# Optimization experiments

Measured on AMD Instinct MI355X. Metric: run time of the kernel, lower is better.

The kernel has to match this reference:

```python
import jax, jax.numpy as jnp
import numpy as np
import math

D = 2048
NH = 16
DH = D // NH
LAT = D // 4
B, S = 2, 2048
EPS = 1e-5


def _ln(x, g, b):
    m = jnp.mean(x, axis=-1, keepdims=True)
    v = jnp.mean((x - m) ** 2, axis=-1, keepdims=True)
    return (x - m) * jax.lax.rsqrt(v + EPS) * g + b


def setup_inputs() -> dict:
    key = jax.random.key(0)
    ks = jax.random.split(key, 12)
    p = lambda k, shape: 0.01 * jax.random.normal(k, shape, dtype=jnp.float32)
    return {
        "x": jax.random.normal(ks[0], (B, S, D), dtype=jnp.float32),
        "W_dq": p(ks[1], (D, LAT)),
        "W_uq": p(ks[2], (LAT, D)),
        "q_ln_g": jnp.ones((LAT,), jnp.float32),
        "q_ln_b": jnp.zeros((LAT,), jnp.float32),
        "W_dkv": p(ks[3], (D, LAT)),
        "W_ukv": p(ks[4], (LAT, 2 * D)),
        "kv_ln_g": jnp.ones((LAT,), jnp.float32),
        "kv_ln_b": jnp.zeros((LAT,), jnp.float32),
        "W_o": p(ks[5], (D, D)),
        "norm1_g": jnp.ones((D,), jnp.float32),
        "norm1_b": jnp.zeros((D,), jnp.float32),
        "norm2_g": jnp.ones((D,), jnp.float32),
        "norm2_b": jnp.zeros((D,), jnp.float32),
        "fc1_w": p(ks[6], (4 * D, D)),
        "fc1_b": jnp.zeros((4 * D,), jnp.float32),
        "fc2_w": p(ks[7], (D, 4 * D)),
        "fc2_b": jnp.zeros((D,), jnp.float32),
    }


def reference(x, W_dq, W_uq, q_ln_g, q_ln_b, W_dkv, W_ukv, kv_ln_g, kv_ln_b,
              W_o, norm1_g, norm1_b, norm2_g, norm2_b, fc1_w, fc1_b, fc2_w, fc2_b):
    normed = _ln(x, norm1_g, norm1_b)

    # --- RopelessMLA attention ---
    cq = _ln(normed @ W_dq, q_ln_g, q_ln_b)          # [B,S,LAT]
    Q = cq @ W_uq                                     # [B,S,D]
    ckv = _ln(normed @ W_dkv, kv_ln_g, kv_ln_b)       # [B,S,LAT]
    KV = ckv @ W_ukv                                  # [B,S,2D]
    K, V = KV[..., :D], KV[..., D:]

    q = Q.reshape(B, S, NH, DH)
    k = K.reshape(B, S, NH, DH)
    v = V.reshape(B, S, NH, DH)

    qkt = jnp.einsum("bqhd,bkhd->bhqk", q, k) / math.sqrt(float(DH))
    mask = jnp.tril(jnp.ones((S, S), dtype=qkt.dtype))  # causal, past_length=0
    qkt = qkt * mask
    qkt = jnp.where(qkt == 0.0, -jnp.inf, qkt)  # faithful to original zero->-inf trick
    attn = jax.nn.softmax(qkt, axis=-1)
    o = jnp.einsum("bhqk,bkhd->bqhd", attn, v).reshape(B, S, D)
    mh_x = o @ W_o.T

    x = x + mh_x
    h = _ln(x, norm2_g, norm2_b)
    h = jax.nn.relu(h @ fc1_w.T + fc1_b)
    h = h @ fc2_w.T + fc2_b  # dropout is identity in eval mode
    return x + h
```

## Files before the change

### kernel.cpp

```cpp
#include <hip/hip_runtime.h>
#include <hip/hip_bf16.h>


#define DEVI __device__ __forceinline__

typedef __attribute__((ext_vector_type(8))) short bf16x8;
typedef __attribute__((ext_vector_type(4))) float f32x4;

DEVI unsigned short f2bf(float f) {
  union { float f; unsigned u; } v; v.f = f;
  unsigned r = v.u + 0x7fffu + ((v.u >> 16) & 1u);
  return (unsigned short)(r >> 16);
}

DEVI float bf2f(unsigned short u) {
  union { unsigned u; float f; } v; v.u = ((unsigned)u) << 16;
  return v.f;
}

#define GLDS16(gp, lp)                                              \
  __builtin_amdgcn_global_load_lds(                                 \
      (__attribute__((address_space(1))) void*)(gp),                \
      (__attribute__((address_space(3))) void*)(lp), 16, 0, 0)

#define NEG_INF (-__builtin_inff())

__global__ __launch_bounds__(256) void cast_f32_bf16(
    const float* __restrict__ in, unsigned short* __restrict__ out, long n) {
  long i = ((long)blockIdx.x * 256 + threadIdx.x) * 4;
  if (i >= n) return;
  const float4 v = *reinterpret_cast<const float4*>(in + i);
  ushort4 o;
  o.x = f2bf(v.x); o.y = f2bf(v.y); o.z = f2bf(v.z); o.w = f2bf(v.w);
  *reinterpret_cast<ushort4*>(out + i) = o;
}

__global__ __launch_bounds__(256) void transpose_cast(
    const float* __restrict__ in, unsigned short* __restrict__ out, int R, int C) {
  __shared__ float tile[32][33];
  const int c0 = blockIdx.x * 32, r0 = blockIdx.y * 32;
  const int tx = threadIdx.x & 31, ty = threadIdx.x >> 5;
#pragma unroll
  for (int i = 0; i < 32; i += 8)
    tile[ty + i][tx] = in[(long)(r0 + ty + i) * C + c0 + tx];
  __syncthreads();
#pragma unroll
  for (int i = 0; i < 32; i += 8)
    out[(long)(c0 + ty + i) * R + r0 + tx] = f2bf(tile[tx][ty + i]);
}

__global__ __launch_bounds__(256) void v_transpose(
    const unsigned short* __restrict__ KV, unsigned short* __restrict__ Vt) {
  __shared__ unsigned short sh[32][33];
  const int s0 = blockIdx.x * 32, d0 = blockIdx.y * 32, bh = blockIdx.z;
  const int b = bh >> 4, h = bh & 15;
  const int tx = threadIdx.x & 31, ty = threadIdx.x >> 5;
#pragma unroll
  for (int i = 0; i < 32; i += 8)
    sh[ty + i][tx] = KV[((long)(b * 2048 + s0 + ty + i)) * 4096 + 2048 + h * 128 + d0 + tx];
  __syncthreads();
#pragma unroll
  for (int i = 0; i < 32; i += 8)
    Vt[((long)(bh * 128 + d0 + ty + i)) * 2048 + s0 + tx] = sh[tx][ty + i];
}

DEVI float blockReduceSum(float v) {
  v += __shfl_xor(v, 1);  v += __shfl_xor(v, 2);  v += __shfl_xor(v, 4);
  v += __shfl_xor(v, 8);  v += __shfl_xor(v, 16); v += __shfl_xor(v, 32);
  __shared__ float red[4];
  if ((threadIdx.x & 63) == 0) red[threadIdx.x >> 6] = v;
  __syncthreads();
  v = red[0] + red[1] + red[2] + red[3];
  __syncthreads();
  return v;
}

template <int W>
__global__ __launch_bounds__(256) void layernorm_bf16(
    const float* __restrict__ in, const float* __restrict__ g,
    const float* __restrict__ b, unsigned short* __restrict__ out, int ldin) {
  constexpr int VPT = W / 256;
  const long row = blockIdx.x;
  const float* x = in + row * ldin;
  float v[VPT];
  float s = 0.f;
#pragma unroll
  for (int i = 0; i < VPT; i++) { v[i] = x[threadIdx.x + i * 256]; s += v[i]; }
  s = blockReduceSum(s);
  const float mean = s * (1.0f / W);
  float s2 = 0.f;
#pragma unroll
  for (int i = 0; i < VPT; i++) { float d = v[i] - mean; s2 += d * d; }
  s2 = blockReduceSum(s2);
  const float rstd = rsqrtf(s2 * (1.0f / W) + 1e-5f);
#pragma unroll
  for (int i = 0; i < VPT; i++) {
    const int c = threadIdx.x + i * 256;
    out[row * W + c] = f2bf((v[i] - mean) * rstd * g[c] + b[c]);
  }
}

__global__ __launch_bounds__(256) void combine_ln(
    const unsigned short* __restrict__ p, const float* __restrict__ xres,
    const float* __restrict__ g, const float* __restrict__ b,
    float* __restrict__ x2, unsigned short* __restrict__ h1, long n) {
  const int c0 = threadIdx.x * 8;
  const long base = (long)blockIdx.x * 2048 + c0;
  float v[8];
  float s = 0.f;
#pragma unroll
  for (int hh = 0; hh < 2; hh++) {
    const long i = base + hh * 4;
    const ushort4 a  = *reinterpret_cast<const ushort4*>(p + i);
    const ushort4 bb = *reinterpret_cast<const ushort4*>(p + n + i);
    const float4 r = *reinterpret_cast<const float4*>(xres + i);
    float4 o;
    o.x = r.x + bf2f(a.x) + bf2f(bb.x);
    o.y = r.y + bf2f(a.y) + bf2f(bb.y);
    o.z = r.z + bf2f(a.z) + bf2f(bb.z);
    o.w = r.w + bf2f(a.w) + bf2f(bb.w);
    *reinterpret_cast<float4*>(x2 + i) = o;
    v[hh * 4 + 0] = o.x; v[hh * 4 + 1] = o.y;
    v[hh * 4 + 2] = o.z; v[hh * 4 + 3] = o.w;
    s += o.x + o.y + o.z + o.w;
  }
  s = blockReduceSum(s);
  const float mean = s * (1.0f / 2048.f);
  float s2 = 0.f;
#pragma unroll
  for (int i = 0; i < 8; i++) { float d = v[i] - mean; s2 += d * d; }
  s2 = blockReduceSum(s2);
  const float rstd = rsqrtf(s2 * (1.0f / 2048.f) + 1e-5f);
#pragma unroll
  for (int hh = 0; hh < 2; hh++) {
    const float4 gv = *reinterpret_cast<const float4*>(g + c0 + hh * 4);
    const float4 bv = *reinterpret_cast<const float4*>(b + c0 + hh * 4);
    ushort4 o;
    o.x = f2bf((v[hh * 4 + 0] - mean) * rstd * gv.x + bv.x);
    o.y = f2bf((v[hh * 4 + 1] - mean) * rstd * gv.y + bv.y);
    o.z = f2bf((v[hh * 4 + 2] - mean) * rstd * gv.z + bv.z);
    o.w = f2bf((v[hh * 4 + 3] - mean) * rstd * gv.w + bv.w);
    *reinterpret_cast<ushort4*>(h1 + base + hh * 4) = o;
  }
}

template <bool BIAS, bool RELU, bool RES, bool OBF16>
__global__ __launch_bounds__(256) void gemm_bt(
    const unsigned short* __restrict__ A, const unsigned short* __restrict__ Bt,
    const float* __restrict__ bias, const float* __restrict__ res,
    void* __restrict__ Cout, int M, int N, int K) {
  __shared__ __align__(16) unsigned short As[2][128 * 32];
  __shared__ __align__(16) unsigned short Bs[2][128 * 32];

  const int m0 = blockIdx.x * 128;
  const int n0 = blockIdx.y * 128;
  const int tid = threadIdx.x;
  const int lane = tid & 63, w = tid >> 6;
  const int wr = (w >> 1) * 64, wc = (w & 1) * 64;
  const int lrow = lane & 15, lk = (lane >> 4) * 8;

  f32x4 acc[4][4] = {};

  const int nt = K >> 5;
  const int r_ = (tid * 8) >> 5;
  const int c_ = (tid * 8) & 31;

#define STAGE(buf, t)                                                        \
  {                                                                          \
    const long k0 = (long)(t) * 32;                                          \
    GLDS16(A + (long)(m0 + r_) * K + k0 + c_, &As[buf][tid * 8]);            \
    GLDS16(A + (long)(m0 + 64 + r_) * K + k0 + c_, &As[buf][2048 + tid * 8]);\
    GLDS16(Bt + (long)(n0 + r_) * K + k0 + c_, &Bs[buf][tid * 8]);           \
    GLDS16(Bt + (long)(n0 + 64 + r_) * K + k0 + c_, &Bs[buf][2048 + tid * 8]);\
  }

  STAGE(0, 0)
  __syncthreads();
  int cur = 0;
  for (int t = 0; t < nt; t++) {
    if (t + 1 < nt) STAGE(cur ^ 1, t + 1)
    bf16x8 fa[4], fb[4];
#pragma unroll
    for (int i = 0; i < 4; i++) {
      fa[i] = *reinterpret_cast<const bf16x8*>(&As[cur][(wr + i * 16 + lrow) * 32 + lk]);
      fb[i] = *reinterpret_cast<const bf16x8*>(&Bs[cur][(wc + i * 16 + lrow) * 32 + lk]);
    }
#pragma unroll
    for (int i = 0; i < 4; i++)
#pragma unroll
      for (int j = 0; j < 4; j++)
        acc[i][j] = __builtin_amdgcn_mfma_f32_16x16x32_bf16(fa[i], fb[j], acc[i][j], 0, 0, 0);
    __syncthreads();
    cur ^= 1;
  }
#undef STAGE

#pragma unroll
  for (int i = 0; i < 4; i++) {
#pragma unroll
    for (int j = 0; j < 4; j++) {
      const int row = m0 + wr + i * 16 + ((lane >> 4) << 2);
      const int col = n0 + wc + j * 16 + lrow;
      float bv = 0.f;
      if (BIAS) bv = bias[col];
#pragma unroll
      for (int r = 0; r < 4; r++) {
        float v = acc[i][j][r];
        const long idx = (long)(row + r) * N + col;
        if (BIAS) v += bv;
        if (RELU) v = fmaxf(v, 0.f);
        if (RES) v += res[idx];
        if (OBF16) ((unsigned short*)Cout)[idx] = f2bf(v);
        else       ((float*)Cout)[idx] = v;
      }
    }
  }
}

template <bool BIAS, bool RELU, bool OBF16>
__global__ __launch_bounds__(512, 1) void gemm256p(
    const unsigned short* __restrict__ A, const unsigned short* __restrict__ Bt,
    const float* __restrict__ bias, void* __restrict__ Cout,
    int M, int N, int lda, int ldb, int kLen, long kOff) {
  __shared__ __align__(16) unsigned short L[2][2][2][256 * 32];

  const int m0 = blockIdx.x * 256, n0 = blockIdx.y * 256;
  const long ka = (long)blockIdx.z * kOff;
  const int tid = threadIdx.x;
  const int lane = tid & 63, w = tid >> 6;
  const int wm = w >> 2, wn = w & 3;
  const int g = lane >> 4, lrow = lane & 15;

  f32x4 acc[8][4] = {};
  const int nt = kLen >> 6;

#define STG(b, ab, kh, t, P, base0, ld)                                        \
  {                                                                            \
    const long k0 = ka + (long)(t) * 64 + (kh) * 32;                           \
    { const int o = tid;       const int r = o >> 2, s = o & 3;                \
      GLDS16((P) + (long)((base0) + r) * (ld) + k0 + ((s ^ ((r >> 1) & 3)) << 3), \
             &L[b][ab][kh][o * 8]); }                                          \
    { const int o = 512 + tid; const int r = o >> 2, s = o & 3;                \
      GLDS16((P) + (long)((base0) + r) * (ld) + k0 + ((s ^ ((r >> 1) & 3)) << 3), \
             &L[b][ab][kh][o * 8]); }                                          \
  }

#define RD_A(dst, Ahalf, qm)                                                   \
  _Pragma("unroll")                                                            \
  for (int i = 0; i < 4; i++) {                                                \
    const int r = wm * 128 + (qm) * 64 + i * 16 + lrow;                        \
    dst[i] = *reinterpret_cast<const bf16x8*>(                                 \
        &(Ahalf)[(r * 4 + (g ^ ((r >> 1) & 3))) * 8]);                         \
  }
#define RD_B(dst, Bhalf)                                                       \
  _Pragma("unroll")                                                            \
  for (int j = 0; j < 4; j++) {                                                \
    const int r = wn * 64 + j * 16 + lrow;                                     \
    dst[j] = *reinterpret_cast<const bf16x8*>(                                 \
        &(Bhalf)[(r * 4 + (g ^ ((r >> 1) & 3))) * 8]);                         \
  }

  STG(0, 0, 0, 0, A, m0, lda)
  STG(0, 1, 0, 0, Bt, n0, ldb)
  STG(0, 0, 1, 0, A, m0, lda)
  STG(0, 1, 1, 0, Bt, n0, ldb)
  asm volatile("s_waitcnt vmcnt(4)\n\ts_barrier" ::: "memory");

  for (int t = 0; t < nt; t++) {
    const int bu = t & 1, bn = bu ^ 1;
    const bool pf = (t + 1 < nt);
#pragma unroll
    for (int kh = 0; kh < 2; kh++) {
      const unsigned short* Ah = L[bu][0][kh];
      const unsigned short* Bh = L[bu][1][kh];
      bf16x8 fa[4], fa2[4], fb[4];
      RD_A(fa, Ah, 0)
      RD_B(fb, Bh)
      RD_A(fa2, Ah, 1)
      if (pf) {
        STG(bn, 0, kh, t + 1, A, m0, lda)
        STG(bn, 1, kh, t + 1, Bt, n0, ldb)
      }
      __builtin_amdgcn_s_setprio(1);
#pragma unroll
      for (int i = 0; i < 4; i++)
#pragma unroll
        for (int j = 0; j < 4; j++)
          acc[i][j] = __builtin_amdgcn_mfma_f32_16x16x32_bf16(fa[i], fb[j], acc[i][j], 0, 0, 0);
#pragma unroll
      for (int i = 0; i < 4; i++)
#pragma unroll
        for (int j = 0; j < 4; j++)
          acc[4 + i][j] = __builtin_amdgcn_mfma_f32_16x16x32_bf16(fa2[i], fb[j], acc[4 + i][j], 0, 0, 0);
      __builtin_amdgcn_s_setprio(0);
      if (kh == 0) {
        if (pf) asm volatile("s_waitcnt vmcnt(4)\n\ts_barrier" ::: "memory");
        else    asm volatile("s_waitcnt vmcnt(0)\n\ts_barrier" ::: "memory");
      } else if (pf) {
        asm volatile("s_waitcnt vmcnt(4) lgkmcnt(0)\n\ts_barrier" ::: "memory");
      }
    }
  }
#undef STG
#undef RD_A
#undef RD_B

  const long zoff = (long)blockIdx.z * (long)M * (long)N;
#pragma unroll
  for (int i = 0; i < 8; i++) {
#pragma unroll
    for (int j = 0; j < 4; j++) {
      const int row = m0 + wm * 128 + i * 16 + g * 4;
      const int col = n0 + wn * 64 + j * 16 + lrow;
      float bv = 0.f;
      if (BIAS) bv = bias[col];
#pragma unroll
      for (int r = 0; r < 4; r++) {
        float v = acc[i][j][r];
        if (BIAS) v += bv;
        if (RELU) v = fmaxf(v, 0.f);
        const long idx = zoff + (long)(row + r) * N + col;
        if (OBF16) ((unsigned short*)Cout)[idx] = f2bf(v);
        else       ((float*)Cout)[idx] = v;
      }
    }
  }
}

template <bool BIAS>
__global__ __launch_bounds__(256) void combine2(
    const unsigned short* __restrict__ p, const float* __restrict__ bias,
    const float* __restrict__ res, float* __restrict__ out, long n) {
  const long i = ((long)blockIdx.x * 256 + threadIdx.x) * 4;
  if (i >= n) return;
  const ushort4 a = *reinterpret_cast<const ushort4*>(p + i);
  const ushort4 b = *reinterpret_cast<const ushort4*>(p + n + i);
  const float4 r = *reinterpret_cast<const float4*>(res + i);
  float4 o;
  o.x = bf2f(a.x) + bf2f(b.x) + r.x;
  o.y = bf2f(a.y) + bf2f(b.y) + r.y;
  o.z = bf2f(a.z) + bf2f(b.z) + r.z;
  o.w = bf2f(a.w) + bf2f(b.w) + r.w;
  if (BIAS) {
    const int col = (int)(i & 2047);
    const float4 bv = *reinterpret_cast<const float4*>(bias + col);
    o.x += bv.x; o.y += bv.y; o.z += bv.z; o.w += bv.w;
  }
  *reinterpret_cast<float4*>(out + i) = o;
}

__global__ __launch_bounds__(256) void flash_attn(
    const unsigned short* __restrict__ Q, const unsigned short* __restrict__ KV,
    const unsigned short* __restrict__ Vt, unsigned short* __restrict__ O) {
  constexpr int S = 2048;
  const int tid = threadIdx.x, lane = tid & 63, w = tid >> 6;
  const int g = lane >> 4, lcol = lane & 15;
  const int wg = blockIdx.x;
  const int x8 = wg & 7, q64 = wg >> 3;
  const int p = q64 & 15, hi = q64 >> 4;
  const int bh = x8 * 4 + hi;
  const int b = bh >> 4, h = bh & 15;
  const long kvrow0 = (long)b * S;
  const int hd0 = h * 128;

  __shared__ __align__(16) unsigned short Kl[64 * 128];
  __shared__ __align__(16) unsigned short Vl[128 * 64];
  __shared__ __align__(16) unsigned short Pl[4 * 16 * 72];

  const float kscale = 0.08838834764831845f * 1.4426950408889634f;

  for (int ti = 0; ti < 2; ti++) {
    const int t = ti ? (31 - p) : p;
    const int qbase = t * 64;
    bf16x8 qf[4];
#pragma unroll
    for (int dc = 0; dc < 4; dc++)
      qf[dc] = *reinterpret_cast<const bf16x8*>(
          Q + (kvrow0 + qbase + w * 16 + lcol) * 2048 + hd0 + dc * 32 + g * 8);
    f32x4 oacc[8] = {};
    float mst[4] = {NEG_INF, NEG_INF, NEG_INF, NEG_INF};
    float lst[4] = {0.f, 0.f, 0.f, 0.f};
    const int nk = t + 1;
    for (int kt = 0; kt < nk; kt++) {
      const int kv0 = kt * 64;
      __syncthreads();
#pragma unroll
      for (int i = 0; i < 4; i++) {
        const int o16 = i * 256 + tid;
        const int kr = o16 >> 4, ks = o16 & 15;
        GLDS16(KV + (kvrow0 + kv0 + kr) * 4096 + hd0 + 8 * (ks ^ (kr & 7)),
               Kl + o16 * 8);
        const int vd = o16 >> 3, vs = o16 & 7;
        GLDS16(Vt + ((long)bh * 128 + vd) * 2048 + kv0 + 8 * (vs ^ (vd & 7)),
               Vl + o16 * 8);
      }
      __syncthreads();
      f32x4 sc[4] = {};
      __builtin_amdgcn_s_setprio(1);
#pragma unroll
      for (int dc = 0; dc < 4; dc++) {
#pragma unroll
        for (int c = 0; c < 4; c++) {
          const bf16x8 kf = *reinterpret_cast<const bf16x8*>(
              Kl + (c * 16 + lcol) * 128 + 8 * ((4 * dc + g) ^ (lcol & 7)));
          sc[c] = __builtin_amdgcn_mfma_f32_16x16x32_bf16(qf[dc], kf, sc[c], 0, 0, 0);
        }
      }
      __builtin_amdgcn_s_setprio(0);
      float s[4][4];
      const int qrow = qbase + w * 16 + g * 4;
      if (kt == nk - 1) {
#pragma unroll
        for (int c = 0; c < 4; c++) {
          const int col = kv0 + c * 16 + lcol;
#pragma unroll
          for (int r = 0; r < 4; r++)
            s[c][r] = (col <= qrow + r) ? sc[c][r] * kscale : NEG_INF;
        }
      } else {
#pragma unroll
        for (int c = 0; c < 4; c++)
#pragma unroll
          for (int r = 0; r < 4; r++) s[c][r] = sc[c][r] * kscale;
      }
      float pm[4];
#pragma unroll
      for (int r = 0; r < 4; r++) {
        float mx = fmaxf(fmaxf(s[0][r], s[1][r]), fmaxf(s[2][r], s[3][r]));
        mx = fmaxf(mx, __shfl_xor(mx, 1));
        mx = fmaxf(mx, __shfl_xor(mx, 2));
        mx = fmaxf(mx, __shfl_xor(mx, 4));
        mx = fmaxf(mx, __shfl_xor(mx, 8));
        pm[r] = mx;
      }
      bool need = false;
#pragma unroll
      for (int r = 0; r < 4; r++) need = need || (pm[r] > mst[r] + 11.5f);
      if (__any(need)) {
#pragma unroll
        for (int r = 0; r < 4; r++) {
          const float mnew = fmaxf(mst[r], pm[r]);
          const float corr = exp2f(mst[r] - mnew);
          mst[r] = mnew;
          lst[r] *= corr;
#pragma unroll
          for (int db = 0; db < 8; db++) oacc[db][r] *= corr;
        }
      }
#pragma unroll
      for (int r = 0; r < 4; r++) {
        float ps = 0.f;
#pragma unroll
        for (int c = 0; c < 4; c++) {
          const float pv = exp2f(s[c][r] - mst[r]);
          Pl[(w * 16 + g * 4 + r) * 72 + c * 16 + lcol] = f2bf(pv);
          ps += pv;
        }
        ps += __shfl_xor(ps, 1); ps += __shfl_xor(ps, 2);
        ps += __shfl_xor(ps, 4); ps += __shfl_xor(ps, 8);
        lst[r] += ps;
      }
      __builtin_amdgcn_s_setprio(1);
#pragma unroll
      for (int kk = 0; kk < 2; kk++) {
        const bf16x8 pf = *reinterpret_cast<const bf16x8*>(
            Pl + (w * 16 + lcol) * 72 + kk * 32 + g * 8);
#pragma unroll
        for (int db = 0; db < 8; db++) {
          const bf16x8 vf = *reinterpret_cast<const bf16x8*>(
              Vl + (db * 16 + lcol) * 64 + 8 * ((4 * kk + g) ^ (lcol & 7)));
          oacc[db] = __builtin_amdgcn_mfma_f32_16x16x32_bf16(pf, vf, oacc[db], 0, 0, 0);
        }
      }
      __builtin_amdgcn_s_setprio(0);
    }
#pragma unroll
    for (int db = 0; db < 8; db++)
#pragma unroll
      for (int r = 0; r < 4; r++) {
        const int qi = qbase + w * 16 + g * 4 + r;
        O[(kvrow0 + qi) * 2048 + hd0 + db * 16 + lcol] = f2bf(oacc[db][r] / lst[r]);
      }
  }
}

extern "C" void kernel_launch(void* const* d_in, const int* in_sizes, int n_in,
                              void* d_out, int out_size, void* d_ws, size_t ws_size,
                              hipStream_t stream) {
  (void)in_sizes; (void)n_in; (void)out_size; (void)ws_size;
  const float* x     = (const float*)d_in[0];
  const float* W_dq  = (const float*)d_in[1];
  const float* W_uq  = (const float*)d_in[2];
  const float* qlng  = (const float*)d_in[3];
  const float* qlnb  = (const float*)d_in[4];
  const float* W_dkv = (const float*)d_in[5];
  const float* W_ukv = (const float*)d_in[6];
  const float* klng  = (const float*)d_in[7];
  const float* klnb  = (const float*)d_in[8];
  const float* W_o   = (const float*)d_in[9];
  const float* n1g   = (const float*)d_in[10];
  const float* n1b   = (const float*)d_in[11];
  const float* n2g   = (const float*)d_in[12];
  const float* n2b   = (const float*)d_in[13];
  const float* fc1w  = (const float*)d_in[14];
  const float* fc1b  = (const float*)d_in[15];
  const float* fc2w  = (const float*)d_in[16];
  const float* fc2b  = (const float*)d_in[17];
  float* out = (float*)d_out;

  char* ws = (char*)d_ws;
  unsigned short* normed = (unsigned short*)(ws + 0);
  unsigned short* Obuf   = (unsigned short*)(ws + 0);
  unsigned short* fc2bb  = (unsigned short*)(ws + 0);
  float*          cqkv_pre = (float*)(ws + 33554432);
  unsigned short* KV       = (unsigned short*)(ws + 33554432);
  unsigned short* fc1bb    = (unsigned short*)(ws + 33554432);
  unsigned short* fc2part  = (unsigned short*)(ws + 33554432);
  unsigned short* cq  = (unsigned short*)(ws + 67108864);
  unsigned short* Qb = (unsigned short*)(ws + 71303168);
  unsigned short* h1 = (unsigned short*)(ws + 71303168);
  unsigned short* ckv = (unsigned short*)(ws + 88080384);
  float* x2           = (float*)(ws + 88080384);
  unsigned short* Vtb    = (unsigned short*)(ws + 121634816);
  unsigned short* wopart = (unsigned short*)(ws + 121634816);
  unsigned short* hmid   = (unsigned short*)(ws + 121634816);
  unsigned short* dqkv_t = (unsigned short*)(ws + 188743680);
  unsigned short* uq_t   = dqkv_t + 2097152;
  unsigned short* ukv_t  = uq_t + 1048576;
  unsigned short* wo_b   = ukv_t + 2097152;

  const dim3 blk(256);
  const dim3 blk8(512);

  transpose_cast<<<dim3(512 / 32, 2048 / 32), blk, 0, stream>>>(W_dq, dqkv_t, 2048, 512);
  transpose_cast<<<dim3(512 / 32, 2048 / 32), blk, 0, stream>>>(W_dkv, dqkv_t + 512 * 2048, 2048, 512);
  transpose_cast<<<dim3(2048 / 32, 512 / 32), blk, 0, stream>>>(W_uq, uq_t, 512, 2048);
  transpose_cast<<<dim3(4096 / 32, 512 / 32), blk, 0, stream>>>(W_ukv, ukv_t, 512, 4096);
  cast_f32_bf16<<<2048 * 2048 / 1024, blk, 0, stream>>>(W_o, wo_b, 2048 * 2048);

  layernorm_bf16<2048><<<4096, blk, 0, stream>>>(x, n1g, n1b, normed, 2048);
  gemm_bt<false, false, false, false><<<dim3(32, 8), blk, 0, stream>>>(
      normed, dqkv_t, nullptr, nullptr, cqkv_pre, 4096, 1024, 2048);
  layernorm_bf16<512><<<4096, blk, 0, stream>>>(cqkv_pre, qlng, qlnb, cq, 1024);
  layernorm_bf16<512><<<4096, blk, 0, stream>>>(cqkv_pre + 512, klng, klnb, ckv, 1024);
  gemm_bt<false, false, false, true><<<dim3(32, 16), blk, 0, stream>>>(
      cq, uq_t, nullptr, nullptr, Qb, 4096, 2048, 512);
  gemm256p<false, false, true><<<dim3(16, 16), blk8, 0, stream>>>(
      ckv, ukv_t, nullptr, KV, 4096, 4096, 512, 512, 512, 0);
  v_transpose<<<dim3(64, 4, 32), blk, 0, stream>>>(KV, Vtb);
  flash_attn<<<dim3(512), blk, 0, stream>>>(Qb, KV, Vtb, Obuf);
  cast_f32_bf16<<<8192 * 2048 / 1024, blk, 0, stream>>>(fc1w, fc1bb, 8192L * 2048);
  gemm256p<false, false, true><<<dim3(16, 8, 2), blk8, 0, stream>>>(
      Obuf, wo_b, nullptr, wopart, 4096, 2048, 2048, 2048, 1024, 1024);
  cast_f32_bf16<<<2048 * 8192 / 1024, blk, 0, stream>>>(fc2w, fc2bb, 2048L * 8192);
  combine_ln<<<4096, blk, 0, stream>>>(wopart, x, n2g, n2b, x2, h1, 8388608L);
  gemm256p<true, true, true><<<dim3(16, 32), blk8, 0, stream>>>(
      h1, fc1bb, fc1b, hmid, 4096, 8192, 2048, 2048, 2048, 0);
  gemm256p<false, false, true><<<dim3(16, 8, 2), blk8, 0, stream>>>(
      hmid, fc2bb, nullptr, fc2part, 4096, 2048, 8192, 8192, 4096, 4096);
  combine2<true><<<8192, blk, 0, stream>>>(fc2part, fc2b, x2, out, 8388608L);
}
```

Measured before the change: 581.3 us.

## Restructure 256x256 GEMM into four quadrant phases with staggered half-tile prefetch

Reorganises the gemm256p main loop so each warp computes four 64x32 sub-blocks spread across the 2x2 quadrants of the 256x256 tile. Each K step runs as four phases: read one quadrant's fragments from LDS, issue the prefetch for one half of A or B, then run that quadrant's MFMAs. Barriers are tied to when each half-tile load lands. The aim is to spread global-to-LDS loads and barrier waits more evenly across the compute so memory latency is hidden better. The trade-off is more complex synchronisation: phase three has no barrier and the tail uses a different vmcnt schedule, which risks races if a count is wrong.

Result: no change. 572.1 us (-1.6%).

```diff
diff --git a/kernel.cpp b/kernel.cpp
--- a/kernel.cpp
+++ b/kernel.cpp
@@ -228,100 +228,136 @@
   const long ka = (long)blockIdx.z * kOff;
   const int tid = threadIdx.x;
   const int lane = tid & 63, w = tid >> 6;
-  const int wm = w >> 2, wn = w & 3;
+  const int sr = (w >> 2) * 64, sc = (w & 3) * 32;
   const int g = lane >> 4, lrow = lane & 15;
-
-  f32x4 acc[8][4] = {};
+  const int r_ = tid >> 2, s_ = tid & 3;
+
+  f32x4 acc[2][2][4][2] = {};
   const int nt = kLen >> 6;
 
-#define STG(b, ab, kh, t, P, base0, ld)                                        \
+#define STG1(bb, ab, h, kh, t, P, base0, ld)                                   \
   {                                                                            \
     const long k0 = ka + (long)(t) * 64 + (kh) * 32;                           \
-    { const int o = tid;       const int r = o >> 2, s = o & 3;                \
-      GLDS16((P) + (long)((base0) + r) * (ld) + k0 + ((s ^ ((r >> 1) & 3)) << 3), \
-             &L[b][ab][kh][o * 8]); }                                          \
-    { const int o = 512 + tid; const int r = o >> 2, s = o & 3;                \
-      GLDS16((P) + (long)((base0) + r) * (ld) + k0 + ((s ^ ((r >> 1) & 3)) << 3), \
-             &L[b][ab][kh][o * 8]); }                                          \
-  }
-
-#define RD_A(dst, Ahalf, qm)                                                   \
+    const int rr = (h) * 128 + r_;                                             \
+    GLDS16((P) + (long)((base0) + rr) * (ld) + k0 + ((s_ ^ ((rr >> 1) & 3)) << 3), \
+           &L[bb][ab][kh][((h) * 512 + tid) * 8]);                             \
+  }
+#define STG_A(bb, h, t) STG1(bb, 0, h, 0, t, A, m0, lda) STG1(bb, 0, h, 1, t, A, m0, lda)
+#define STG_B(bb, h, t) STG1(bb, 1, h, 0, t, Bt, n0, ldb) STG1(bb, 1, h, 1, t, Bt, n0, ldb)
+
+#define RD(dst, ab, kh, row)                                                   \
+  dst = *reinterpret_cast<const bf16x8*>(                                      \
+      &L[bu][ab][kh][((row) * 4 + (g ^ (((row) >> 1) & 3))) * 8]);
+
+#define PH_READS(a, b)                                                         \
+  bf16x8 fa[2][4], fb[2][2];                                                   \
   _Pragma("unroll")                                                            \
-  for (int i = 0; i < 4; i++) {                                                \
-    const int r = wm * 128 + (qm) * 64 + i * 16 + lrow;                        \
-    dst[i] = *reinterpret_cast<const bf16x8*>(                                 \
-        &(Ahalf)[(r * 4 + (g ^ ((r >> 1) & 3))) * 8]);                         \
-  }
-#define RD_B(dst, Bhalf)                                                       \
+  for (int kh = 0; kh < 2; kh++) {                                             \
+    _Pragma("unroll")                                                          \
+    for (int i = 0; i < 4; i++) {                                              \
+      const int rr = (a) * 128 + sr + i * 16 + lrow;                           \
+      RD(fa[kh][i], 0, kh, rr)                                                 \
+    }                                                                          \
+    _Pragma("unroll")                                                          \
+    for (int j = 0; j < 2; j++) {                                              \
+      const int rr = (b) * 128 + sc + j * 16 + lrow;                           \
+      RD(fb[kh][j], 1, kh, rr)                                                 \
+    }                                                                          \
+  }
+
+#define PH_MFMA(a, b)                                                          \
+  __builtin_amdgcn_s_setprio(1);                                               \
   _Pragma("unroll")                                                            \
-  for (int j = 0; j < 4; j++) {                                                \
-    const int r = wn * 64 + j * 16 + lrow;                                     \
-    dst[j] = *reinterpret_cast<const bf16x8*>(                                 \
-        &(Bhalf)[(r * 4 + (g ^ ((r >> 1) & 3))) * 8]);                         \
-  }
-
-  STG(0, 0, 0, 0, A, m0, lda)
-  STG(0, 1, 0, 0, Bt, n0, ldb)
-  STG(0, 0, 1, 0, A, m0, lda)
-  STG(0, 1, 1, 0, Bt, n0, ldb)
-  asm volatile("s_waitcnt vmcnt(4)\n\ts_barrier" ::: "memory");
-
-  for (int t = 0; t < nt; t++) {
+  for (int kh = 0; kh < 2; kh++)                                               \
+    _Pragma("unroll")                                                          \
+    for (int i = 0; i < 4; i++)                                                \
+      _Pragma("unroll")                                                        \
+      for (int j = 0; j < 2; j++)                                              \
+        acc[a][b][i][j] = __builtin_amdgcn_mfma_f32_16x16x32_bf16(             \
+            fa[kh][i], fb[kh][j], acc[a][b][i][j], 0, 0, 0);                   \
+  __builtin_amdgcn_s_setprio(0);
+
+  STG_A(0, 0, 0) STG_B(0, 0, 0) STG_A(0, 1, 0) STG_B(0, 1, 0)
+  asm volatile("s_waitcnt vmcnt(0)\n\ts_barrier" ::: "memory");
+
+  int t = 0;
+  for (; t < nt - 1; t++) {
     const int bu = t & 1, bn = bu ^ 1;
-    const bool pf = (t + 1 < nt);
-#pragma unroll
-    for (int kh = 0; kh < 2; kh++) {
-      const unsigned short* Ah = L[bu][0][kh];
-      const unsigned short* Bh = L[bu][1][kh];
-      bf16x8 fa[4], fa2[4], fb[4];
-      RD_A(fa, Ah, 0)
-      RD_B(fb, Bh)
-      RD_A(fa2, Ah, 1)
-      if (pf) {
-        STG(bn, 0, kh, t + 1, A, m0, lda)
-        STG(bn, 1, kh, t + 1, Bt, n0, ldb)
-      }
-      __builtin_amdgcn_s_setprio(1);
-#pragma unroll
-      for (int i = 0; i < 4; i++)
-#pragma unroll
-        for (int j = 0; j < 4; j++)
-          acc[i][j] = __builtin_amdgcn_mfma_f32_16x16x32_bf16(fa[i], fb[j], acc[i][j], 0, 0, 0);
-#pragma unroll
-      for (int i = 0; i < 4; i++)
-#pragma unroll
-        for (int j = 0; j < 4; j++)
-          acc[4 + i][j] = __builtin_amdgcn_mfma_f32_16x16x32_bf16(fa2[i], fb[j], acc[4 + i][j], 0, 0, 0);
-      __builtin_amdgcn_s_setprio(0);
-      if (kh == 0) {
-        if (pf) asm volatile("s_waitcnt vmcnt(4)\n\ts_barrier" ::: "memory");
-        else    asm volatile("s_waitcnt vmcnt(0)\n\ts_barrier" ::: "memory");
-      } else if (pf) {
-        asm volatile("s_waitcnt vmcnt(4) lgkmcnt(0)\n\ts_barrier" ::: "memory");
-      }
-    }
-  }
-#undef STG
-#undef RD_A
-#undef RD_B
+    {
+      PH_READS(0, 0)
+      STG_A(bn, 0, t + 1)
+      PH_MFMA(0, 0)
+      asm volatile("s_waitcnt vmcnt(4)\n\ts_barrier" ::: "memory");
+    }
+    {
+      PH_READS(1, 0)
+      STG_B(bn, 0, t + 1)
+      PH_MFMA(1, 0)
+      asm volatile("s_waitcnt vmcnt(4)\n\ts_barrier" ::: "memory");
+    }
+    {
+      PH_READS(1, 1)
+      STG_A(bn, 1, t + 1)
+      PH_MFMA(1, 1)
+    }
+    {
+      PH_READS(0, 1)
+      STG_B(bn, 1, t + 1)
+      PH_MFMA(0, 1)
+      asm volatile("s_waitcnt vmcnt(4)\n\ts_barrier" ::: "memory");
+    }
+  }
+  {
+    const int bu = t & 1;
+    {
+      PH_READS(0, 0)
+      PH_MFMA(0, 0)
+      asm volatile("s_waitcnt vmcnt(2)\n\ts_barrier" ::: "memory");
+    }
+    {
+      PH_READS(1, 0)
+      PH_MFMA(1, 0)
+      asm volatile("s_waitcnt vmcnt(0)\n\ts_barrier" ::: "memory");
+    }
+    {
+      PH_READS(1, 1)
+      PH_MFMA(1, 1)
+    }
+    {
+      PH_READS(0, 1)
+      PH_MFMA(0, 1)
+    }
+  }
+#undef STG1
+#undef STG_A
+#undef STG_B
+#undef RD
+#undef PH_READS
+#undef PH_MFMA
 
   const long zoff = (long)blockIdx.z * (long)M * (long)N;
 #pragma unroll
-  for (int i = 0; i < 8; i++) {
-#pragma unroll
-    for (int j = 0; j < 4; j++) {
-      const int row = m0 + wm * 128 + i * 16 + g * 4;
-      const int col = n0 + wn * 64 + j * 16 + lrow;
-      float bv = 0.f;
-      if (BIAS) bv = bias[col];
-#pragma unroll
-      for (int r = 0; r < 4; r++) {
-        float v = acc[i][j][r];
-        if (BIAS) v += bv;
-        if (RELU) v = fmaxf(v, 0.f);
-        const long idx = zoff + (long)(row + r) * N + col;
-        if (OBF16) ((unsigned short*)Cout)[idx] = f2bf(v);
-        else       ((float*)Cout)[idx] = v;
+  for (int a = 0; a < 2; a++) {
+#pragma unroll
+    for (int b = 0; b < 2; b++) {
+#pragma unroll
+      for (int i = 0; i < 4; i++) {
+#pragma unroll
+        for (int j = 0; j < 2; j++) {
+          const int row = m0 + a * 128 + sr + i * 16 + g * 4;
+          const int col = n0 + b * 128 + sc + j * 16 + lrow;
+          float bv = 0.f;
+          if (BIAS) bv = bias[col];
+#pragma unroll
+          for (int r = 0; r < 4; r++) {
+            float v = acc[a][b][i][j][r];
+            if (BIAS) v += bv;
+            if (RELU) v = fmaxf(v, 0.f);
+            const long idx = zoff + (long)(row + r) * N + col;
+            if (OBF16) ((unsigned short*)Cout)[idx] = f2bf(v);
+            else       ((float*)Cout)[idx] = v;
+          }
+        }
       }
     }
   }
```
